# Kernel tuning notes

Measured on AMD Instinct MI355X. Metric: run time of the kernel, lower is better.

Reference implementation:

```python
import jax, jax.numpy as jnp
import numpy as np

HIDDEN = 4096
INTER = 11008
BATCH, SEQ = 2, 2048


def setup_inputs() -> dict:
    key = jax.random.key(0)
    ks = jax.random.split(key, 7)
    s_h = 1.0 / np.sqrt(HIDDEN)   # nn.Linear default init bound fan_in=HIDDEN
    s_i = 1.0 / np.sqrt(INTER)    # fan_in=INTER for down_proj
    return {
        "hidden_states": jax.random.normal(ks[0], (BATCH, SEQ, HIDDEN), dtype=jnp.float32),
        "w_gate": jax.random.uniform(ks[1], (INTER, HIDDEN), jnp.float32, -s_h, s_h),
        "b_gate": jax.random.uniform(ks[2], (INTER,), jnp.float32, -s_h, s_h),
        "w_up": jax.random.uniform(ks[3], (INTER, HIDDEN), jnp.float32, -s_h, s_h),
        "b_up": jax.random.uniform(ks[4], (INTER,), jnp.float32, -s_h, s_h),
        "w_down": jax.random.uniform(ks[5], (HIDDEN, INTER), jnp.float32, -s_i, s_i),
        "b_down": jax.random.uniform(ks[6], (HIDDEN,), jnp.float32, -s_i, s_i),
    }


def reference(hidden_states, w_gate, b_gate, w_up, b_up, w_down, b_down):
    # SwiGLU MLP: down( silu(gate(x)) * up(x) )
    gate = jax.nn.silu(jnp.einsum("bsh,ih->bsi", hidden_states, w_gate) + b_gate)
    up = jnp.einsum("bsh,ih->bsi", hidden_states, w_up) + b_up
    return jnp.einsum("bsi,hi->bsh", gate * up, w_down) + b_down
```

## Files before the change

### kernel.cpp

```cpp
#include <hip/hip_runtime.h>
#include <hip/hip_bf16.h>


#define M_TOK 4096
#define HID   4096
#define INT_  11008
#define NGU   1376
#define NCVT  128

typedef __attribute__((ext_vector_type(8))) short bf16x8;
typedef __attribute__((ext_vector_type(4))) float f32x4;
typedef __attribute__((ext_vector_type(16))) float f32x16;

__device__ __forceinline__ unsigned short f2bf(float f) {
    union { float f; unsigned int u; } a; a.f = f;
    unsigned int u = a.u;
    u += 0x7fff + ((u >> 16) & 1);
    return (unsigned short)(u >> 16);
}

__global__ void cvt3(const float* __restrict__ x,  unsigned short* __restrict__ xb,
                     const float* __restrict__ wg, unsigned short* __restrict__ s1,
                     const float* __restrict__ wu, unsigned short* __restrict__ s2,
                     int n4x, int n4w) {
    const int total = n4x + 2 * n4w;
    const int stride = gridDim.x * blockDim.x;
    for (int i = blockIdx.x * blockDim.x + threadIdx.x; i < total; i += stride) {
        const float* src; unsigned short* dst; int j;
        if (i < n4x)            { j = i;             src = x;  dst = xb; }
        else if (i < n4x + n4w) { j = i - n4x;       src = wg; dst = s1; }
        else                    { j = i - n4x - n4w; src = wu; dst = s2; }
        float4 v = ((const float4*)src)[j];
        ushort4 o;
        o.x = f2bf(v.x); o.y = f2bf(v.y); o.z = f2bf(v.z); o.w = f2bf(v.w);
        ((ushort4*)dst)[j] = o;
    }
}

__global__ void cvt_f32_bf16(const float* __restrict__ in, unsigned short* __restrict__ out, int n4) {
    int stride = gridDim.x * blockDim.x;
    for (int i = blockIdx.x * blockDim.x + threadIdx.x; i < n4; i += stride) {
        float4 v = ((const float4*)in)[i];
        ushort4 o;
        o.x = f2bf(v.x); o.y = f2bf(v.y); o.z = f2bf(v.z); o.w = f2bf(v.w);
        ((ushort4*)out)[i] = o;
    }
}

#define GLL(gsrc, ldst) \
    __builtin_amdgcn_global_load_lds( \
        (__attribute__((address_space(1))) void*)(gsrc), \
        (__attribute__((address_space(3))) void*)(ldst), 16, 0, 0)

#define VMC(n) asm volatile("s_waitcnt vmcnt(" #n ")" ::: "memory")
#define BARR __builtin_amdgcn_s_barrier()
#define PIN  __builtin_amdgcn_sched_barrier(0)

#define ZERO16(V) { _Pragma("unroll") for (int z_ = 0; z_ < 16; ++z_) V[z_] = 0.f; }

__global__ __launch_bounds__(512, 2)
void gemm_gu(const unsigned short* __restrict__ A,
             const unsigned short* __restrict__ Wg,
             const unsigned short* __restrict__ Wu,
             const float* __restrict__ bg,
             const float* __restrict__ bu,
             unsigned short* __restrict__ T,
             const float* __restrict__ wdSrc,
             unsigned short* __restrict__ wdDst,
             int M, int NI, int K) {
    __shared__ unsigned short lds[2 * 32768];

    const int tid  = threadIdx.x;

    if (blockIdx.x >= NGU) {
        const int c = blockIdx.x - NGU;
        const size_t base = (size_t)c * 88064;
        const float4* src = (const float4*)wdSrc + base;
        ushort4* dst = (ushort4*)wdDst + base;
#pragma unroll 4
        for (int it = 0; it < 172; ++it) {
            const int u = it * 512 + tid;
            float4 v = src[u];
            ushort4 o;
            o.x = f2bf(v.x); o.y = f2bf(v.y); o.z = f2bf(v.z); o.w = f2bf(v.w);
            dst[u] = o;
        }
        return;
    }

    const int lane = tid & 63;
    const int w    = tid >> 6;
    const int wm   = w >> 2;
    const int wn   = w & 3;

    const int ntn = NI >> 7;
    const int chunk = NGU >> 3;
    const int sw = (blockIdx.x & 7) * chunk + (blockIdx.x >> 3);
    const int bm = sw / ntn, bn = sw % ntn;

    const unsigned short* Ag  = A  + (size_t)(bm * 256) * K;
    const unsigned short* Bgg = Wg + (size_t)(bn * 128) * K;
    const unsigned short* Bug = Wu + (size_t)(bn * 128) * K;

    int offA[2][2], offBW[2];
#pragma unroll
    for (int i = 0; i < 2; ++i) {
        int sig = i * 512 + tid;
        int r   = sig >> 3;
        int s   = (sig & 7) ^ (r & 7);
#pragma unroll
        for (int h = 0; h < 2; ++h) {
            int grow = ((r >> 6) * 2 + h) * 64 + (r & 63);
            offA[h][i] = grow * K + s * 8;
        }
        offBW[i] = r * K + s * 8;
    }

    const int l31 = lane & 31;
    const int hi  = lane >> 5;
    const int x7  = l31 & 7;
    const int aBase = (wm * 64 + l31) * 64;
    const int gBase = 16384 + (wn * 32 + l31) * 64;
    const int uBase = 24576 + (wn * 32 + l31) * 64;
    int slt[4];
#pragma unroll
    for (int kk = 0; kk < 4; ++kk) slt[kk] = ((kk * 2 + hi) ^ x7) * 8;

    f32x16 accg[4], accu[4];
#pragma unroll
    for (int mb = 0; mb < 4; ++mb) { ZERO16(accg[mb]); ZERO16(accu[mb]); }

    const int NT = K >> 6;

#define STAGE_A(H, DST, SRC) \
    GLL((SRC) + offA[H][0], (DST) + (H) * 8192 + tid * 8); \
    GLL((SRC) + offA[H][1], (DST) + (H) * 8192 + 4096 + tid * 8)
#define STAGE_W(BASE, DST, SRC) \
    GLL((SRC) + offBW[0], (DST) + (BASE) + tid * 8); \
    GLL((SRC) + offBW[1], (DST) + (BASE) + 4096 + tid * 8)

#define RD_A32(BUF, QM, DST) \
    { _Pragma("unroll") for (int mb2 = 0; mb2 < 2; ++mb2) \
      _Pragma("unroll") for (int kk = 0; kk < 4; ++kk) \
        DST[mb2 * 4 + kk] = *(const bf16x8*)((BUF) + (QM) * 8192 + aBase + mb2 * 2048 + slt[kk]); }
#define RD_W32(BUF, BASE, DST) \
    { _Pragma("unroll") for (int kk = 0; kk < 4; ++kk) \
        DST[kk] = *(const bf16x8*)((BUF) + (BASE) + slt[kk]); }
#define Q8(ACC, MB0, AF, BF) \
    { _Pragma("unroll") for (int mb2 = 0; mb2 < 2; ++mb2) \
      _Pragma("unroll") for (int kk = 0; kk < 4; ++kk) \
        ACC[(MB0) + mb2] = __builtin_amdgcn_mfma_f32_32x32x16_bf16( \
            AF[mb2 * 4 + kk], BF[kk], ACC[(MB0) + mb2], 0, 0, 0); }

    bf16x8 A0f[8], A1f[8], Bgf[4], Buf_[4];

    STAGE_A(0, lds, Ag);
    STAGE_W(16384, lds, Bgg);
    STAGE_W(24576, lds, Bug);
    STAGE_A(1, lds, Ag);
    VMC(2);
    BARR; PIN;

    for (int t = 0; t < NT; ++t) {
        const unsigned short* bc = lds + (t & 1) * 32768;
        unsigned short* sb = lds + ((t + 1) & 1) * 32768;
        const int ts = (t + 1 < NT) ? (t + 1) : (NT - 1);
        const unsigned short* sA = Ag + (size_t)ts * 64;
        const unsigned short* sG = Bgg + (size_t)ts * 64;
        const unsigned short* sU = Bug + (size_t)ts * 64;

        RD_A32(bc, 0, A0f);
        RD_W32(bc, gBase, Bgf);
        STAGE_A(0, sb, sA);
        Q8(accg, 0, A0f, Bgf);
        RD_W32(bc, uBase, Buf_);
        STAGE_W(16384, sb, sG);
        Q8(accu, 0, A0f, Buf_);
        STAGE_W(24576, sb, sU);
        VMC(6);
        BARR; PIN;

        RD_A32(bc, 1, A1f);
        STAGE_A(1, sb, sA);
        Q8(accg, 2, A1f, Bgf);
        Q8(accu, 2, A1f, Buf_);
        VMC(2);
        BARR; PIN;
    }
#undef RD_A32
#undef RD_W32
#undef Q8
#undef STAGE_A
#undef STAGE_W

    const int rowW = bm * 256 + wm * 128;
    const int col  = bn * 128 + wn * 32 + l31;
    const float bgv = bg[col];
    const float buv = bu[col];
#pragma unroll
    for (int mb = 0; mb < 4; ++mb) {
#pragma unroll
        for (int reg = 0; reg < 16; ++reg) {
            const int row = rowW + mb * 32 + (reg & 3) + ((reg >> 2) << 3) + (hi << 2);
            float g = accg[mb][reg] + bgv;
            float u = accu[mb][reg] + buv;
            float s = g / (1.f + __expf(-g)) * u;
            T[(size_t)row * (size_t)INT_ + col] = f2bf(s);
        }
    }
}

__global__ __launch_bounds__(512, 2)
void gemm_dn(const unsigned short* __restrict__ A,
             const unsigned short* __restrict__ B,
             const float* __restrict__ bias,
             float* __restrict__ C,
             int M, int N, int K) {
    __shared__ unsigned short lds[2 * 32768];

    const int tid  = threadIdx.x;
    const int lane = tid & 63;
    const int w    = tid >> 6;
    const int wm   = w >> 2;
    const int wn   = w & 3;

    const int ntn = N >> 8;
    const int chunk = gridDim.x >> 3;
    const int sw = (blockIdx.x & 7) * chunk + (blockIdx.x >> 3);
    const int bm = sw / ntn, bn = sw % ntn;

    const unsigned short* Ag = A + (size_t)(bm * 256) * K;
    const unsigned short* Bg = B + (size_t)(bn * 256) * K;

    int offA[2][2], offB[2][2];
#pragma unroll
    for (int h = 0; h < 2; ++h)
#pragma unroll
        for (int i = 0; i < 2; ++i) {
            int sig = i * 512 + tid;
            int r   = sig >> 3;
            int s   = (sig & 7) ^ (r & 7);
            int grow = ((r >> 6) * 2 + h) * 64 + (r & 63);
            int gcol = ((r >> 5) * 2 + h) * 32 + (r & 31);
            offA[h][i] = grow * K + s * 8;
            offB[h][i] = gcol * K + s * 8;
        }

    const int l31 = lane & 31;
    const int hi  = lane >> 5;
    const int x7  = l31 & 7;
    const int aBase = (wm * 64 + l31) * 64;
    const int bBase = 16384 + (wn * 32 + l31) * 64;
    int slt[4];
#pragma unroll
    for (int kk = 0; kk < 4; ++kk) slt[kk] = ((kk * 2 + hi) ^ x7) * 8;

    f32x16 acc[4][2];
#pragma unroll
    for (int mb = 0; mb < 4; ++mb) { ZERO16(acc[mb][0]); ZERO16(acc[mb][1]); }

    const int NT = K >> 6;

#define STAGE_A(H, DST, SRC) \
    GLL((SRC) + offA[H][0], (DST) + (H) * 8192 + tid * 8); \
    GLL((SRC) + offA[H][1], (DST) + (H) * 8192 + 4096 + tid * 8)
#define STAGE_B(H, DST, SRC) \
    GLL((SRC) + offB[H][0], (DST) + 16384 + (H) * 8192 + tid * 8); \
    GLL((SRC) + offB[H][1], (DST) + 16384 + (H) * 8192 + 4096 + tid * 8)
#define RD_A32(BUF, QM, DST) \
    { _Pragma("unroll") for (int mb2 = 0; mb2 < 2; ++mb2) \
      _Pragma("unroll") for (int kk = 0; kk < 4; ++kk) \
        DST[mb2 * 4 + kk] = *(const bf16x8*)((BUF) + (QM) * 8192 + aBase + mb2 * 2048 + slt[kk]); }
#define RD_B32(BUF, QN, DST) \
    { _Pragma("unroll") for (int kk = 0; kk < 4; ++kk) \
        DST[kk] = *(const bf16x8*)((BUF) + (QN) * 8192 + bBase + slt[kk]); }
#define Q8D(MB0, QN, AF, BF) \
    { _Pragma("unroll") for (int mb2 = 0; mb2 < 2; ++mb2) \
      _Pragma("unroll") for (int kk = 0; kk < 4; ++kk) \
        acc[(MB0) + mb2][QN] = __builtin_amdgcn_mfma_f32_32x32x16_bf16( \
            AF[mb2 * 4 + kk], BF[kk], acc[(MB0) + mb2][QN], 0, 0, 0); }

    bf16x8 A0f[8], A1f[8], B0f[4], B1f[4];

    STAGE_A(0, lds, Ag); STAGE_B(0, lds, Bg); STAGE_B(1, lds, Bg); STAGE_A(1, lds, Ag);
    VMC(2);
    BARR; PIN;

    for (int t = 0; t < NT; ++t) {
        const unsigned short* bc = lds + (t & 1) * 32768;
        unsigned short* sb = lds + ((t + 1) & 1) * 32768;
        const int ts = (t + 1 < NT) ? (t + 1) : (NT - 1);
        const unsigned short* sAt = Ag + (size_t)ts * 64;
        const unsigned short* sBt = Bg + (size_t)ts * 64;

        RD_A32(bc, 0, A0f);
        RD_B32(bc, 0, B0f);
        STAGE_A(0, sb, sAt);
        Q8D(0, 0, A0f, B0f);
        RD_B32(bc, 1, B1f);
        STAGE_B(0, sb, sBt);
        Q8D(0, 1, A0f, B1f);
        STAGE_B(1, sb, sBt);
        VMC(6);
        BARR; PIN;

        RD_A32(bc, 1, A1f);
        STAGE_A(1, sb, sAt);
        Q8D(2, 1, A1f, B1f);
        Q8D(2, 0, A1f, B0f);
        VMC(2);
        BARR; PIN;
    }
#undef RD_A32
#undef RD_B32
#undef Q8D
#undef STAGE_A
#undef STAGE_B

    const int rowW = bm * 256 + wm * 128;
#pragma unroll
    for (int mb = 0; mb < 4; ++mb)
#pragma unroll
        for (int qn = 0; qn < 2; ++qn) {
            const int col = bn * 256 + wn * 64 + qn * 32 + l31;
            const float bv = bias[col];
#pragma unroll
            for (int reg = 0; reg < 16; ++reg) {
                const int row = rowW + mb * 32 + (reg & 3) + ((reg >> 2) << 3) + (hi << 2);
                C[(size_t)row * (size_t)N + col] = acc[mb][qn][reg] + bv;
            }
        }
}

extern "C" void kernel_launch(void* const* d_in, const int* in_sizes, int n_in,
                              void* d_out, int out_size, void* d_ws, size_t ws_size,
                              hipStream_t stream) {
    const float* x  = (const float*)d_in[0];
    const float* wg = (const float*)d_in[1];
    const float* bg = (const float*)d_in[2];
    const float* wu = (const float*)d_in[3];
    const float* bu = (const float*)d_in[4];
    const float* wd = (const float*)d_in[5];
    const float* bd = (const float*)d_in[6];

    const size_t NX = (size_t)M_TOK * HID;
    const size_t NW = (size_t)INT_ * HID;

    unsigned short* ws = (unsigned short*)d_ws;
    unsigned short* Xb = ws;
    unsigned short* S1 = Xb + NX;
    unsigned short* S2 = S1 + NW;
    unsigned short* S3 = S2 + NW;
    unsigned short* S4 = S3 + NW;

    const bool fused = ws_size >= (NX + 4 * NW) * 2;

    dim3 blk512(512);
    dim3 blk256(256);

    cvt3<<<2048, blk256, 0, stream>>>(x, Xb, wg, S1, wu, S2,
                                      (int)(NX / 4), (int)(NW / 4));

    if (fused) {
        gemm_gu<<<dim3(NGU + NCVT), blk512, 0, stream>>>(Xb, S1, S2, bg, bu, S3,
                                                         wd, S4, M_TOK, INT_, HID);
        gemm_dn<<<dim3(16 * 16), blk512, 0, stream>>>(S3, S4, bd, (float*)d_out,
                                                      M_TOK, HID, INT_);
    } else {
        gemm_gu<<<dim3(NGU), blk512, 0, stream>>>(Xb, S1, S2, bg, bu, S3,
                                                  (const float*)nullptr,
                                                  (unsigned short*)nullptr,
                                                  M_TOK, INT_, HID);
        cvt_f32_bf16<<<2048, blk256, 0, stream>>>(wd, S1, (int)(NW / 4));
        gemm_dn<<<dim3(16 * 16), blk512, 0, stream>>>(S3, S1, bd, (float*)d_out,
                                                      M_TOK, HID, INT_);
    }
}
```

Measured before the change: 1.117 ms.

## Replace XOR-swizzled LDS layout with fragment-ordered staging for MFMA reads

Both GEMM kernels now compute global-to-LDS staging offsets so tiles land in LDS already in MFMA fragment order, letting each lane read its fragments with a simple linear offset instead of XOR-swizzled slots. The aim is to cut LDS bank conflicts and address arithmetic on fragment reads. The down GEMM also changes which N columns each wave owns, and the epilogue column mapping is updated to match. The cost is less contiguous global loads (16-byte pieces spread over many rows), which may reduce coalescing.

Measured after the change: 1.189 ms. 6.5% more time.

```diff
diff --git a/kernel.cpp b/kernel.cpp
--- a/kernel.cpp
+++ b/kernel.cpp
@@ -58,6 +58,7 @@
 
 #define ZERO16(V) { _Pragma("unroll") for (int z_ = 0; z_ < 16; ++z_) V[z_] = 0.f; }
 
+
 __global__ __launch_bounds__(512, 2)
 void gemm_gu(const unsigned short* __restrict__ A,
              const unsigned short* __restrict__ Wg,
@@ -102,29 +103,27 @@
     const unsigned short* Bgg = Wg + (size_t)(bn * 128) * K;
     const unsigned short* Bug = Wu + (size_t)(bn * 128) * K;
 
-    int offA[2][2], offBW[2];
-#pragma unroll
-    for (int i = 0; i < 2; ++i) {
-        int sig = i * 512 + tid;
-        int r   = sig >> 3;
-        int s   = (sig & 7) ^ (r & 7);
-#pragma unroll
-        for (int h = 0; h < 2; ++h) {
-            int grow = ((r >> 6) * 2 + h) * 64 + (r & 63);
-            offA[h][i] = grow * K + s * 8;
-        }
-        offBW[i] = r * K + s * 8;
-    }
+    int gOffA[2][2], gOffW[2];
+#pragma unroll
+    for (int h = 0; h < 2; ++h)
+#pragma unroll
+        for (int g = 0; g < 2; ++g) {
+            int c   = g * 512 + tid;
+            int wmD = c >> 9, j = (c >> 8) & 1;
+            int kk  = (c >> 6) & 3;
+            int q   = (c >> 2) & 15, hh = (c >> 1) & 1, o = c & 1;
+            int row = wmD * 128 + (h * 2 + j) * 32 + hh * 16 + q;
+            int k   = kk * 16 + o * 8;
+            gOffA[h][g] = row * K + k;
+            if (h == 0) {
+                int colB = ((c >> 8) & 3) * 32 + hh * 16 + q;
+                gOffW[g] = colB * K + k;
+            }
+        }
 
     const int l31 = lane & 31;
     const int hi  = lane >> 5;
-    const int x7  = l31 & 7;
-    const int aBase = (wm * 64 + l31) * 64;
-    const int gBase = 16384 + (wn * 32 + l31) * 64;
-    const int uBase = 24576 + (wn * 32 + l31) * 64;
-    int slt[4];
-#pragma unroll
-    for (int kk = 0; kk < 4; ++kk) slt[kk] = ((kk * 2 + hi) ^ x7) * 8;
+    const int aLane = (l31 & 15) * 32 + ((l31 >> 4) & 1) * 16 + hi * 8;
 
     f32x16 accg[4], accu[4];
 #pragma unroll
@@ -133,19 +132,19 @@
     const int NT = K >> 6;
 
 #define STAGE_A(H, DST, SRC) \
-    GLL((SRC) + offA[H][0], (DST) + (H) * 8192 + tid * 8); \
-    GLL((SRC) + offA[H][1], (DST) + (H) * 8192 + 4096 + tid * 8)
+    GLL((SRC) + gOffA[H][0], (DST) + (H) * 8192 + tid * 8); \
+    GLL((SRC) + gOffA[H][1], (DST) + (H) * 8192 + 4096 + tid * 8)
 #define STAGE_W(BASE, DST, SRC) \
-    GLL((SRC) + offBW[0], (DST) + (BASE) + tid * 8); \
-    GLL((SRC) + offBW[1], (DST) + (BASE) + 4096 + tid * 8)
-
-#define RD_A32(BUF, QM, DST) \
+    GLL((SRC) + gOffW[0], (DST) + (BASE) + tid * 8); \
+    GLL((SRC) + gOffW[1], (DST) + (BASE) + 4096 + tid * 8)
+
+#define RD_A32(BUF, HALF, DST) \
     { _Pragma("unroll") for (int mb2 = 0; mb2 < 2; ++mb2) \
       _Pragma("unroll") for (int kk = 0; kk < 4; ++kk) \
-        DST[mb2 * 4 + kk] = *(const bf16x8*)((BUF) + (QM) * 8192 + aBase + mb2 * 2048 + slt[kk]); }
+        DST[mb2 * 4 + kk] = *(const bf16x8*)((BUF) + (HALF) * 8192 + wm * 4096 + mb2 * 2048 + kk * 512 + aLane); }
 #define RD_W32(BUF, BASE, DST) \
     { _Pragma("unroll") for (int kk = 0; kk < 4; ++kk) \
-        DST[kk] = *(const bf16x8*)((BUF) + (BASE) + slt[kk]); }
+        DST[kk] = *(const bf16x8*)((BUF) + (BASE) + wn * 2048 + kk * 512 + aLane); }
 #define Q8(ACC, MB0, AF, BF) \
     { _Pragma("unroll") for (int mb2 = 0; mb2 < 2; ++mb2) \
       _Pragma("unroll") for (int kk = 0; kk < 4; ++kk) \
@@ -170,10 +169,10 @@
         const unsigned short* sU = Bug + (size_t)ts * 64;
 
         RD_A32(bc, 0, A0f);
-        RD_W32(bc, gBase, Bgf);
+        RD_W32(bc, 16384, Bgf);
         STAGE_A(0, sb, sA);
         Q8(accg, 0, A0f, Bgf);
-        RD_W32(bc, uBase, Buf_);
+        RD_W32(bc, 24576, Buf_);
         STAGE_W(16384, sb, sG);
         Q8(accu, 0, A0f, Buf_);
         STAGE_W(24576, sb, sU);
@@ -232,28 +231,25 @@
     const unsigned short* Ag = A + (size_t)(bm * 256) * K;
     const unsigned short* Bg = B + (size_t)(bn * 256) * K;
 
-    int offA[2][2], offB[2][2];
+    int gOffA[2][2], gOffB[2][2];
 #pragma unroll
     for (int h = 0; h < 2; ++h)
 #pragma unroll
-        for (int i = 0; i < 2; ++i) {
-            int sig = i * 512 + tid;
-            int r   = sig >> 3;
-            int s   = (sig & 7) ^ (r & 7);
-            int grow = ((r >> 6) * 2 + h) * 64 + (r & 63);
-            int gcol = ((r >> 5) * 2 + h) * 32 + (r & 31);
-            offA[h][i] = grow * K + s * 8;
-            offB[h][i] = gcol * K + s * 8;
+        for (int g = 0; g < 2; ++g) {
+            int c   = g * 512 + tid;
+            int wmD = c >> 9, j = (c >> 8) & 1;
+            int kk  = (c >> 6) & 3;
+            int q   = (c >> 2) & 15, hh = (c >> 1) & 1, o = c & 1;
+            int row = wmD * 128 + (h * 2 + j) * 32 + hh * 16 + q;
+            int k   = kk * 16 + o * 8;
+            gOffA[h][g] = row * K + k;
+            int colB = (h * 4 + ((c >> 8) & 3)) * 32 + hh * 16 + q;
+            gOffB[h][g] = colB * K + k;
         }
 
     const int l31 = lane & 31;
     const int hi  = lane >> 5;
-    const int x7  = l31 & 7;
-    const int aBase = (wm * 64 + l31) * 64;
-    const int bBase = 16384 + (wn * 32 + l31) * 64;
-    int slt[4];
-#pragma unroll
-    for (int kk = 0; kk < 4; ++kk) slt[kk] = ((kk * 2 + hi) ^ x7) * 8;
+    const int aLane = (l31 & 15) * 32 + ((l31 >> 4) & 1) * 16 + hi * 8;
 
     f32x16 acc[4][2];
 #pragma unroll
@@ -262,18 +258,18 @@
     const int NT = K >> 6;
 
 #define STAGE_A(H, DST, SRC) \
-    GLL((SRC) + offA[H][0], (DST) + (H) * 8192 + tid * 8); \
-    GLL((SRC) + offA[H][1], (DST) + (H) * 8192 + 4096 + tid * 8)
+    GLL((SRC) + gOffA[H][0], (DST) + (H) * 8192 + tid * 8); \
+    GLL((SRC) + gOffA[H][1], (DST) + (H) * 8192 + 4096 + tid * 8)
 #define STAGE_B(H, DST, SRC) \
-    GLL((SRC) + offB[H][0], (DST) + 16384 + (H) * 8192 + tid * 8); \
-    GLL((SRC) + offB[H][1], (DST) + 16384 + (H) * 8192 + 4096 + tid * 8)
-#define RD_A32(BUF, QM, DST) \
+    GLL((SRC) + gOffB[H][0], (DST) + 16384 + (H) * 8192 + tid * 8); \
+    GLL((SRC) + gOffB[H][1], (DST) + 16384 + (H) * 8192 + 4096 + tid * 8)
+#define RD_A32(BUF, HALF, DST) \
     { _Pragma("unroll") for (int mb2 = 0; mb2 < 2; ++mb2) \
       _Pragma("unroll") for (int kk = 0; kk < 4; ++kk) \
-        DST[mb2 * 4 + kk] = *(const bf16x8*)((BUF) + (QM) * 8192 + aBase + mb2 * 2048 + slt[kk]); }
+        DST[mb2 * 4 + kk] = *(const bf16x8*)((BUF) + (HALF) * 8192 + wm * 4096 + mb2 * 2048 + kk * 512 + aLane); }
 #define RD_B32(BUF, QN, DST) \
     { _Pragma("unroll") for (int kk = 0; kk < 4; ++kk) \
-        DST[kk] = *(const bf16x8*)((BUF) + (QN) * 8192 + bBase + slt[kk]); }
+        DST[kk] = *(const bf16x8*)((BUF) + 16384 + ((QN) * 4 + wn) * 2048 + kk * 512 + aLane); }
 #define Q8D(MB0, QN, AF, BF) \
     { _Pragma("unroll") for (int mb2 = 0; mb2 < 2; ++mb2) \
       _Pragma("unroll") for (int kk = 0; kk < 4; ++kk) \
@@ -322,7 +318,7 @@
     for (int mb = 0; mb < 4; ++mb)
 #pragma unroll
         for (int qn = 0; qn < 2; ++qn) {
-            const int col = bn * 256 + wn * 64 + qn * 32 + l31;
+            const int col = bn * 256 + qn * 128 + wn * 32 + l31;
             const float bv = bias[col];
 #pragma unroll
             for (int reg = 0; reg < 16; ++reg) {
```
